# Optimization experiments

Measured on AMD Instinct MI355X. Metric: run time of the kernel, lower is better.

The kernel has to match this reference:

```python
import jax, jax.numpy as jnp
import numpy as np

NT = 3            # node types
NET = 9           # edge types = all ordered pairs
PAIR_A = np.repeat(np.arange(NT), NT)   # et[0].value per edge type
PAIR_B = np.tile(np.arange(NT), NT)     # et[1].value per edge type


def setup_inputs() -> dict:
    key = jax.random.key(0)
    ks = jax.random.split(key, 20)
    bs, Na, Nc, CS, D, H, Z = 8, 128, 256, 3, 64, 64, 8
    s = 0.05
    inp = {
        'node_types': jax.random.randint(ks[0], (bs, Na), 0, NT),
        'node_enc': jax.random.normal(ks[1], (bs, Na, D), dtype=jnp.float32),
        'edge_enc': jax.random.normal(ks[2], (bs, Na, Na, 1, D), dtype=jnp.float32),
        'clique_index': jax.random.randint(ks[3], (bs, Nc), 0, Na),
        'clique_node_index': jax.random.randint(ks[4], (bs, Nc, CS), 0, Na),
        'clique_order_index': jax.random.randint(ks[5], (bs, Nc, CS), 0, CS),
        # per-node-type MLP params (stacked over type axis)
        'nW0': jax.random.normal(ks[6], (NT, D, H)) * s, 'nb0': jnp.zeros((NT, H)),
        'nW1': jax.random.normal(ks[7], (NT, H, H)) * s, 'nb1': jnp.zeros((NT, H)),
        'nW2': jax.random.normal(ks[8], (NT, H, Z)) * s, 'nb2': jnp.zeros((NT, Z)),
        # per-edge-type MLP params
        'eW0': jax.random.normal(ks[9], (NET, D, H)) * s, 'eb0': jnp.zeros((NET, H)),
        'eW1': jax.random.normal(ks[10], (NET, H, H)) * s, 'eb1': jnp.zeros((NET, H)),
        'eW2': jax.random.normal(ks[11], (NET, H, Z * Z)) * s, 'eb2': jnp.zeros((NET, Z * Z)),
    }
    return inp


def reference(node_types, node_enc, edge_enc, clique_index, clique_node_index,
              clique_order_index, nW0, nb0, nW1, nb1, nW2, nb2,
              eW0, eb0, eW1, eb1, eW2, eb2):
    bs, Na = node_types.shape
    Nc, cs = clique_node_index.shape[1:]
    Z = nb2.shape[-1]

    # ---- node factors: dense per-type MLP then type-mask accumulate ----
    h = jax.nn.relu(jnp.einsum('bnd,tdh->tbnh', node_enc, nW0) + nb0[:, None, None, :])
    h = jax.nn.relu(jnp.einsum('tbnh,thk->tbnk', h, nW1) + nb1[:, None, None, :])
    nf_all = jnp.einsum('tbnk,tkz->tbnz', h, nW2) + nb2[:, None, None, :]  # [T,bs,Na,Z]
    nmask = (node_types[None] == jnp.arange(NT)[:, None, None]).astype(nf_all.dtype)
    node_factor = jnp.einsum('tbnz,tbn->bnz', nf_all, nmask)  # [bs,Na,Z]

    # ---- edge factors: last timestep of edge_enc, per-pair-type MLP + mask ----
    e = edge_enc[..., -1, :]  # [bs,Na,Na,D]
    h = jax.nn.relu(jnp.einsum('bijd,tdh->tbijh', e, eW0) + eb0[:, None, None, None, :])
    h = jax.nn.relu(jnp.einsum('tbijh,thk->tbijk', h, eW1) + eb1[:, None, None, None, :])
    ef_all = jnp.einsum('tbijk,tkz->tbijz', h, eW2) + eb2[:, None, None, None, :]  # [9,bs,Na,Na,Z*Z]
    pa = jnp.asarray(PAIR_A)
    pb = jnp.asarray(PAIR_B)
    # et_flag[b,i,j] = (types[b,j]==et0) & (types[b,i]==et1)  (matches torch unsqueeze(1)/(2))
    emask = ((node_types[None, :, None, :] == pa[:, None, None, None]) &
             (node_types[None, :, :, None] == pb[:, None, None, None])).astype(ef_all.dtype)
    edge_factor = jnp.einsum('tbijz,tbij->bijz', ef_all, emask).reshape(bs, Na, Na, Z, Z)

    # ---- pad with zero row/col for index -1 sentinel ----
    nfe = jnp.pad(node_factor, ((0, 0), (0, 1), (0, 0)))                     # [bs,Na+1,Z]
    efe = jnp.pad(edge_factor, ((0, 0), (0, 1), (0, 1), (0, 0), (0, 0)))
    efe_flat = efe.reshape(bs, (Na + 1) * (Na + 1), Z, Z)

    idx = jnp.where(clique_node_index < 0, Na, clique_node_index)  # [bs,Nc,cs]
    b_ix = jnp.arange(bs)[:, None, None]
    nfc = nfe[b_ix, idx]  # [bs,Nc,cs,Z]

    logpi = jnp.zeros((bs, Nc) + (Z,) * cs, node_factor.dtype)
    for i in range(cs):
        shape = (bs, Nc) + (1,) * i + (Z,) + (1,) * (cs - 1 - i)
        logpi = logpi + nfc[:, :, i, :].reshape(shape)
    b2 = jnp.arange(bs)[:, None]
    for i in range(cs - 1):
        for j in range(i + 1, cs):
            fl = idx[:, :, i] * (Na + 1) + idx[:, :, j]          # [bs,Nc]
            ef_ij = efe_flat[b2, fl]                              # [bs,Nc,Z,Z]
            shape = (bs, Nc) + (1,) * i + (Z,) + (1,) * (j - i - 1) + (Z,) + (1,) * (cs - 1 - j)
            logpi = logpi + ef_ij.reshape(shape)

    z = jnp.stack(jnp.meshgrid(*([jnp.arange(Z)] * cs), indexing='ij'), -1)
    return logpi, z
```

## Files before the change

kernel.cpp:

```cpp
#include <hip/hip_runtime.h>
#include <hip/hip_bf16.h>


#define BS   8
#define NA   128
#define NC   256
#define DIM  64
#define ZZ   8

__global__ __launch_bounds__(64) void node_mlp_kernel(
    const int* __restrict__ nt, const float* __restrict__ enc,
    const float* __restrict__ W0, const float* __restrict__ b0,
    const float* __restrict__ W1, const float* __restrict__ b1,
    const float* __restrict__ W2, const float* __restrict__ b2,
    float* __restrict__ nf ) {
  const int blk  = blockIdx.x;
  const int lane = threadIdx.x;
  const int t = nt[blk];

  float e = enc[blk * DIM + lane];

  float acc = b0[t * DIM + lane];
  {
    const float* w = W0 + t * DIM * DIM + lane;
#pragma unroll
    for (int k = 0; k < DIM; ++k) acc = fmaf(__shfl(e, k), w[k * DIM], acc);
  }
  float h = fmaxf(acc, 0.f);

  acc = b1[t * DIM + lane];
  {
    const float* w = W1 + t * DIM * DIM + lane;
#pragma unroll
    for (int k = 0; k < DIM; ++k) acc = fmaf(__shfl(h, k), w[k * DIM], acc);
  }
  float h1 = fmaxf(acc, 0.f);

  const int z = lane & 7, s = lane >> 3;
  acc = 0.f;
  {
    const float* w2 = W2 + t * DIM * ZZ + z;
#pragma unroll
    for (int k = 0; k < 8; ++k)
      acc = fmaf(__shfl(h1, s * 8 + k), w2[(s * 8 + k) * ZZ], acc);
  }
  acc += __shfl_xor(acc, 8);
  acc += __shfl_xor(acc, 16);
  acc += __shfl_xor(acc, 32);
  if (lane < ZZ) nf[blk * ZZ + lane] = acc + b2[t * ZZ + lane];
}

__global__ __launch_bounds__(256) void clique_fused_kernel(
    const int* __restrict__ nt, const int* __restrict__ cni,
    const float* __restrict__ edge_enc, const float* __restrict__ nf,
    const float* __restrict__ eW0, const float* __restrict__ eb0,
    const float* __restrict__ eW1, const float* __restrict__ eb1,
    const float* __restrict__ eW2, const float* __restrict__ eb2,
    float* __restrict__ out) {
  const int blk  = blockIdx.x;
  const int tid  = threadIdx.x;
  const int wave = tid >> 6, lane = tid & 63;
  const int b = blk >> 8;

  __shared__ int   idxs[3];
  __shared__ float nfs[3][ZZ];
  __shared__ float ef[3][DIM];

  if (tid < 3) {
    int v = cni[blk * 3 + tid];
    idxs[tid] = (v < 0 || v >= NA) ? NA : v;
  }
  __syncthreads();

  if (wave == 3) {
    if (lane < 3 * ZZ) {
      const int i = lane >> 3, z = lane & 7, v = idxs[i];
      nfs[i][z] = (v < NA) ? nf[(b * NA + v) * ZZ + z] : 0.f;
    }
  } else {
    const int p = wave;
    const int pi = (p == 2) ? 1 : 0;
    const int pj = (p == 0) ? 1 : 2;
    const int ia = idxs[pi], jb = idxs[pj];
    if (ia >= NA || jb >= NA) {
      ef[p][lane] = 0.f;
    } else {
      const int t = nt[b * NA + jb] * 3 + nt[b * NA + ia];
      float e = edge_enc[((b * NA + ia) * NA + jb) * DIM + lane];

      float acc = eb0[t * DIM + lane];
      {
        const float* w = eW0 + t * DIM * DIM + lane;
#pragma unroll
        for (int k = 0; k < DIM; ++k) acc = fmaf(__shfl(e, k), w[k * DIM], acc);
      }
      e = fmaxf(acc, 0.f);

      acc = eb1[t * DIM + lane];
      {
        const float* w = eW1 + t * DIM * DIM + lane;
#pragma unroll
        for (int k = 0; k < DIM; ++k) acc = fmaf(__shfl(e, k), w[k * DIM], acc);
      }
      e = fmaxf(acc, 0.f);

      acc = eb2[t * DIM + lane];
      {
        const float* w = eW2 + t * DIM * DIM + lane;
#pragma unroll
        for (int k = 0; k < DIM; ++k) acc = fmaf(__shfl(e, k), w[k * DIM], acc);
      }
      ef[p][lane] = acc;
    }
  }
  __syncthreads();

  if (wave == 0) {
    const int z1 = lane >> 3, z2 = lane & 7;
    const float base = nfs[1][z1] + nfs[2][z2] + ef[2][z1 * ZZ + z2];
    float* o = out + blk * (ZZ * ZZ * ZZ);
#pragma unroll
    for (int z0 = 0; z0 < ZZ; ++z0) {
      o[z0 * 64 + lane] = base + nfs[0][z0] + ef[0][z0 * ZZ + z1] + ef[1][z0 * ZZ + z2];
    }
  } else if (wave == 1 && blk < 24) {
    const int i = blk * 64 + lane;
    const int k = i % 3;
    const int r = i / 3;
    const int zz2 = r & 7, zz1 = (r >> 3) & 7, zz0 = r >> 6;
    const int v = (k == 0) ? zz0 : ((k == 1) ? zz1 : zz2);
    out[BS * NC * ZZ * ZZ * ZZ + i] = (float)v;
  }
}

extern "C" void kernel_launch(void* const* d_in, const int* in_sizes, int n_in,
                              void* d_out, int out_size, void* d_ws, size_t ws_size,
                              hipStream_t stream) {
  const int*   node_types = (const int*)  d_in[0];
  const float* node_enc   = (const float*)d_in[1];
  const float* edge_enc   = (const float*)d_in[2];
  const int*   cni        = (const int*)  d_in[4];
  const float* nW0 = (const float*)d_in[6];
  const float* nb0 = (const float*)d_in[7];
  const float* nW1 = (const float*)d_in[8];
  const float* nb1 = (const float*)d_in[9];
  const float* nW2 = (const float*)d_in[10];
  const float* nb2 = (const float*)d_in[11];
  const float* eW0 = (const float*)d_in[12];
  const float* eb0 = (const float*)d_in[13];
  const float* eW1 = (const float*)d_in[14];
  const float* eb1 = (const float*)d_in[15];
  const float* eW2 = (const float*)d_in[16];
  const float* eb2 = (const float*)d_in[17];

  float* out = (float*)d_out;
  float* node_factor = (float*)d_ws;

  node_mlp_kernel<<<BS * NA, 64, 0, stream>>>(
      node_types, node_enc, nW0, nb0, nW1, nb1, nW2, nb2, node_factor);

  clique_fused_kernel<<<BS * NC, 256, 0, stream>>>(
      node_types, cni, edge_enc, node_factor,
      eW0, eb0, eW1, eb1, eW2, eb2, out);
}
```

Before: 128.0 us.

## Fuse node MLP into clique kernel, recomputing node factors per clique

Removes the separate node MLP kernel and its workspace round trip by having each of the three waves in a clique block compute the node MLP for one clique member before its edge MLP. This drops one kernel launch and the inter-kernel dependency. In exchange, node factors are recomputed redundantly for every clique reference and each wave's serial work roughly doubles.

```diff
diff --git a/kernel.cpp b/kernel.cpp
--- a/kernel.cpp
+++ b/kernel.cpp
@@ -8,51 +8,12 @@
 #define DIM  64
 #define ZZ   8
 
-__global__ __launch_bounds__(64) void node_mlp_kernel(
-    const int* __restrict__ nt, const float* __restrict__ enc,
-    const float* __restrict__ W0, const float* __restrict__ b0,
-    const float* __restrict__ W1, const float* __restrict__ b1,
-    const float* __restrict__ W2, const float* __restrict__ b2,
-    float* __restrict__ nf ) {
-  const int blk  = blockIdx.x;
-  const int lane = threadIdx.x;
-  const int t = nt[blk];
-
-  float e = enc[blk * DIM + lane];
-
-  float acc = b0[t * DIM + lane];
-  {
-    const float* w = W0 + t * DIM * DIM + lane;
-#pragma unroll
-    for (int k = 0; k < DIM; ++k) acc = fmaf(__shfl(e, k), w[k * DIM], acc);
-  }
-  float h = fmaxf(acc, 0.f);
-
-  acc = b1[t * DIM + lane];
-  {
-    const float* w = W1 + t * DIM * DIM + lane;
-#pragma unroll
-    for (int k = 0; k < DIM; ++k) acc = fmaf(__shfl(h, k), w[k * DIM], acc);
-  }
-  float h1 = fmaxf(acc, 0.f);
-
-  const int z = lane & 7, s = lane >> 3;
-  acc = 0.f;
-  {
-    const float* w2 = W2 + t * DIM * ZZ + z;
-#pragma unroll
-    for (int k = 0; k < 8; ++k)
-      acc = fmaf(__shfl(h1, s * 8 + k), w2[(s * 8 + k) * ZZ], acc);
-  }
-  acc += __shfl_xor(acc, 8);
-  acc += __shfl_xor(acc, 16);
-  acc += __shfl_xor(acc, 32);
-  if (lane < ZZ) nf[blk * ZZ + lane] = acc + b2[t * ZZ + lane];
-}
-
-__global__ __launch_bounds__(256) void clique_fused_kernel(
+__global__ __launch_bounds__(192) void clique_fused_all(
     const int* __restrict__ nt, const int* __restrict__ cni,
-    const float* __restrict__ edge_enc, const float* __restrict__ nf,
+    const float* __restrict__ node_enc, const float* __restrict__ edge_enc,
+    const float* __restrict__ nW0, const float* __restrict__ nb0,
+    const float* __restrict__ nW1, const float* __restrict__ nb1,
+    const float* __restrict__ nW2, const float* __restrict__ nb2,
     const float* __restrict__ eW0, const float* __restrict__ eb0,
     const float* __restrict__ eW1, const float* __restrict__ eb1,
     const float* __restrict__ eW2, const float* __restrict__ eb2,
@@ -72,13 +33,47 @@
   }
   __syncthreads();
 
-  if (wave == 3) {
-    if (lane < 3 * ZZ) {
-      const int i = lane >> 3, z = lane & 7, v = idxs[i];
-      nfs[i][z] = (v < NA) ? nf[(b * NA + v) * ZZ + z] : 0.f;
+  {
+    const int v = idxs[wave];
+    if (v >= NA) {
+      if (lane < ZZ) nfs[wave][lane] = 0.f;
+    } else {
+      const int t = nt[b * NA + v];
+      float e = node_enc[(b * NA + v) * DIM + lane];
+
+      float acc = nb0[t * DIM + lane];
+      {
+        const float* w = nW0 + t * DIM * DIM + lane;
+#pragma unroll
+        for (int k = 0; k < DIM; ++k) acc = fmaf(__shfl(e, k), w[k * DIM], acc);
+      }
+      e = fmaxf(acc, 0.f);
+
+      acc = nb1[t * DIM + lane];
+      {
+        const float* w = nW1 + t * DIM * DIM + lane;
+#pragma unroll
+        for (int k = 0; k < DIM; ++k) acc = fmaf(__shfl(e, k), w[k * DIM], acc);
+      }
+      e = fmaxf(acc, 0.f);
+
+      const int z = lane & 7, s = lane >> 3;
+      acc = 0.f;
+      {
+        const float* w2 = nW2 + t * DIM * ZZ + z;
+#pragma unroll
+        for (int k = 0; k < 8; ++k)
+          acc = fmaf(__shfl(e, s * 8 + k), w2[(s * 8 + k) * ZZ], acc);
+      }
+      acc += __shfl_xor(acc, 8);
+      acc += __shfl_xor(acc, 16);
+      acc += __shfl_xor(acc, 32);
+      if (lane < ZZ) nfs[wave][lane] = acc + nb2[t * ZZ + lane];
     }
-  } else {
-    const int p = wave;
+  }
+
+  {
+    const int p  = wave;
     const int pi = (p == 2) ? 1 : 0;
     const int pj = (p == 0) ? 1 : 2;
     const int ia = idxs[pi], jb = idxs[pj];
@@ -154,12 +149,9 @@
   const float* eb2 = (const float*)d_in[17];
 
   float* out = (float*)d_out;
-  float* node_factor = (float*)d_ws;
 
-  node_mlp_kernel<<<BS * NA, 64, 0, stream>>>(
-      node_types, node_enc, nW0, nb0, nW1, nb1, nW2, nb2, node_factor);
-
-  clique_fused_kernel<<<BS * NC, 256, 0, stream>>>(
-      node_types, cni, edge_enc, node_factor,
+  clique_fused_all<<<BS * NC, 192, 0, stream>>>(
+      node_types, cni, node_enc, edge_enc,
+      nW0, nb0, nW1, nb1, nW2, nb2,
       eW0, eb0, eW1, eb1, eW2, eb2, out);
 }
```

After: 134.2 us. +4.8%, slower.
